# Kernel tuning notes

Hardware: AMD Instinct MI355X
Metric: run time of the kernel (lower is better)

## Reference

```python
import jax, jax.numpy as jnp
import numpy as np

N_HEADS = 16
HEAD_DIM = 64
ROPE_BASE = 10000.0


def _apply_rope(x, offset):
    # x: (B, T, H, hd); rotates consecutive pairs (x[2i], x[2i+1]) as complex numbers,
    # matching torch.view_as_complex on reshape(..., -1, 2).
    B, T, H, hd = x.shape
    inv_freq = 1.0 / (ROPE_BASE ** (jnp.arange(0, hd, 2, dtype=jnp.float32) / hd))  # (hd/2,)
    t = jnp.arange(T, dtype=jnp.float32) + offset
    ang = t[:, None] * inv_freq[None, :]                      # (T, hd/2)
    cos = jnp.cos(ang)[None, :, None, :]                      # (1, T, 1, hd/2)
    sin = jnp.sin(ang)[None, :, None, :]
    x1 = x[..., 0::2]
    x2 = x[..., 1::2]
    out = jnp.stack([x1 * cos - x2 * sin, x1 * sin + x2 * cos], axis=-1)
    return out.reshape(B, T, H, hd).astype(x.dtype)


def setup_inputs() -> dict:
    key = jax.random.key(0)
    ks = jax.random.split(key, 5)
    D = N_HEADS * HEAD_DIM  # 1024
    s = 1.0 / np.sqrt(D)
    x = jax.random.normal(ks[0], (2, 2048, D), jnp.float32)
    Wqkv = jax.random.normal(ks[1], (D, 3 * D), jnp.float32) * s
    bqkv = jax.random.normal(ks[2], (3 * D,), jnp.float32) * 0.01
    Wout = jax.random.normal(ks[3], (D, D), jnp.float32) * s
    bout = jax.random.normal(ks[4], (D,), jnp.float32) * 0.01
    return {"x": x, "Wqkv": Wqkv, "bqkv": bqkv, "Wout": Wout, "bout": bout, "offset": 0}


def reference(x, Wqkv, bqkv, Wout, bout, offset):
    B, T, D = x.shape
    qkv = (x @ Wqkv + bqkv).reshape(B, T, 3, N_HEADS, HEAD_DIM)
    q, k, v = qkv[:, :, 0], qkv[:, :, 1], qkv[:, :, 2]       # (B, T, H, hd)
    q = _apply_rope(q, offset)
    k = _apply_rope(k, offset)
    # kv_cache is None and T == window_size, so no crop occurs.
    new_cache = jnp.stack([k, v], axis=1)                     # (B, 2, T, H, hd)
    scale = 1.0 / np.sqrt(HEAD_DIM)
    scores = jnp.einsum("bqhd,bkhd->bhqk", q, k) * scale      # (B, H, T, T)
    mask = jnp.tril(jnp.ones((T, T), dtype=bool))
    scores = jnp.where(mask[None, None], scores, jnp.finfo(scores.dtype).min)
    attn = jax.nn.softmax(scores, axis=-1)
    ctx = jnp.einsum("bhqk,bkhd->bqhd", attn, v).reshape(B, T, D)
    out = ctx @ Wout + bout
    return (out, new_cache)
```

## Files before the change

### kernel.cpp

```cpp
#include <hip/hip_runtime.h>
#include <stdint.h>
#include <math.h>


typedef __bf16 bf16_t;
typedef bf16_t bf16x8 __attribute__((ext_vector_type(8)));
typedef float f32x4 __attribute__((ext_vector_type(4)));
typedef unsigned short ushort8_t __attribute__((ext_vector_type(8)));

__device__ __forceinline__ unsigned short f2bf(float f) {
    union { float f; unsigned int i; } v; v.f = f;
    unsigned int r = v.i + 0x7fffu + ((v.i >> 16) & 1u);
    return (unsigned short)(r >> 16);
}
__device__ __forceinline__ bf16x8 ld8(const unsigned short* p) {
    return *(const bf16x8*)p;
}
__device__ __forceinline__ void gload_lds16(const unsigned short* g, unsigned short* l) {
    __builtin_amdgcn_global_load_lds(
        (__attribute__((address_space(1))) void*)(g),
        (__attribute__((address_space(3))) void*)(l),
        16, 0, 0);
}
#define WAITN(n) asm volatile("s_waitcnt vmcnt(" #n ")" ::: "memory")

__global__ void k_cvt(const float* __restrict__ in, unsigned short* __restrict__ out) {
    const int i = (blockIdx.x * 256 + threadIdx.x) * 8;
    float4 a = *(const float4*)&in[i];
    float4 b = *(const float4*)&in[i + 4];
    ushort8_t v;
    v[0] = f2bf(a.x); v[1] = f2bf(a.y); v[2] = f2bf(a.z); v[3] = f2bf(a.w);
    v[4] = f2bf(b.x); v[5] = f2bf(b.y); v[6] = f2bf(b.z); v[7] = f2bf(b.w);
    *(ushort8_t*)&out[i] = v;
}

__global__ void k_ropetab(float* __restrict__ tab, const int* __restrict__ offp) {
    int idx = blockIdx.x * blockDim.x + threadIdx.x;
    int t = idx >> 5, i = idx & 31;
    float off = (float)(*offp);
    float inv = powf(10000.0f, -(float)(2 * i) / 64.0f);
    float ang = ((float)t + off) * inv;
    float s, c;
    sincosf(ang, &s, &c);
    tab[idx * 2]     = c;
    tab[idx * 2 + 1] = s;
}

__global__ void k_transposeF2B(const float* __restrict__ in,
                               unsigned short* __restrict__ out, int R, int C) {
    __shared__ __align__(16) float tile[64 * 68];
    const int bz = blockIdx.z;
    const size_t base = (size_t)bz * R * C;
    const int tR = blockIdx.y * 64, tC = blockIdx.x * 64;
    const int tid = threadIdx.x;
#pragma unroll
    for (int it = 0; it < 4; ++it) {
        int flat = (it * 256 + tid) * 4;
        int r = flat >> 6, c = flat & 63;
        *(float4*)&tile[r * 68 + c] =
            *(const float4*)&in[base + (size_t)(tR + r) * C + tC + c];
    }
    __syncthreads();
#pragma unroll
    for (int it = 0; it < 2; ++it) {
        int flat = (it * 256 + tid) * 8;
        int rr = flat >> 6, cc = flat & 63;
        ushort8_t v;
#pragma unroll
        for (int j = 0; j < 8; ++j) v[j] = f2bf(tile[(cc + j) * 68 + rr]);
        *(ushort8_t*)&out[base + (size_t)(tC + rr) * R + tR + cc] = v;
    }
}

__global__ void k_transpose64(const unsigned short* __restrict__ in,
                              unsigned short* __restrict__ out, int R, int C) {
    __shared__ __align__(16) unsigned short tile[64 * 72];
    const int bz = blockIdx.z;
    const size_t base = (size_t)bz * R * C;
    const int tR = blockIdx.y * 64, tC = blockIdx.x * 64;
    const int tid = threadIdx.x;
#pragma unroll
    for (int it = 0; it < 2; ++it) {
        int flat = (it * 256 + tid) * 8;
        int r = flat >> 6, c = flat & 63;
        *(ushort8_t*)&tile[r * 72 + c] =
            *(const ushort8_t*)&in[base + (size_t)(tR + r) * C + tC + c];
    }
    __syncthreads();
#pragma unroll
    for (int it = 0; it < 2; ++it) {
        int flat = (it * 256 + tid) * 8;
        int rr = flat >> 6, cc = flat & 63;
        ushort8_t v;
#pragma unroll
        for (int j = 0; j < 8; ++j) v[j] = tile[(cc + j) * 72 + rr];
        *(ushort8_t*)&out[base + (size_t)(tC + rr) * R + tR + cc] = v;
    }
}

template <int EPI>
__global__ __launch_bounds__(512, 2) void k_gemm(
    const unsigned short* __restrict__ A,
    const unsigned short* __restrict__ Bt,
    const float* __restrict__ bias,
    const float* __restrict__ tab,
    unsigned short* __restrict__ oq,
    unsigned short* __restrict__ ok,
    unsigned short* __restrict__ ov,
    float* __restrict__ cache,
    float* __restrict__ outp)
{
    constexpr int K = 1024;
    __shared__ __align__(16) unsigned short lds[65536];
    unsigned short* lA = lds;
    unsigned short* lB = lds + 32768;

    const int tid  = threadIdx.x;
    const int lane = tid & 63, w = tid >> 6;
    const int wr = w >> 2, wc = w & 3;
    const int lrow = lane & 15, quad = lane >> 4;

    const int gx  = gridDim.x;
    const int nwg = gx * gridDim.y;
    const int bid = blockIdx.y * gx + blockIdx.x;
    const int sw  = (bid & 7) * (nwg >> 3) + (bid >> 3);
    const int blockM = (sw / gx) * 256;
    const int blockN = (sw % gx) * 256;

    const int q8    = (lane & 7) ^ (lane >> 3);
    const int srow0 = ((w * 16 + (lane >> 3)) << 1) + ((q8 >> 2) & 1);
    const int scol  = (q8 & 3) * 8;
    const unsigned short* srcA = A  + (size_t)(blockM + srow0) * K + scol;
    const unsigned short* srcB = Bt + (size_t)(blockN + srow0) * K + scol;
    unsigned short* dA = lA + w * 1024;
    unsigned short* dB = lB + w * 1024;

    const int rp   = lrow >> 1;
    const int swzu = ((((lane & 1) << 6) | (quad << 4)) ^ (rp << 4)) >> 1;

    f32x4 acc[8][4];
#pragma unroll
    for (int m = 0; m < 8; ++m)
#pragma unroll
        for (int n = 0; n < 4; ++n) acc[m][n] = (f32x4){0.f, 0.f, 0.f, 0.f};

#define STAGE_A(T, KH) do { \
        const unsigned short* s_ = srcA + (T) * 64 + (KH) * 32; \
        unsigned short* d_ = dA + (((2*(T)+(KH)) & 3) << 13); \
        gload_lds16(s_, d_); \
        gload_lds16(s_ + 16 * K, d_ + 512); } while (0)
#define STAGE_B(T, KH) do { \
        const unsigned short* s_ = srcB + (T) * 64 + (KH) * 32; \
        unsigned short* d_ = dB + (((2*(T)+(KH)) & 3) << 13); \
        gload_lds16(s_, d_); \
        gload_lds16(s_ + 16 * K, d_ + 512); } while (0)
#define RD_A(slot) do { \
        _Pragma("unroll") \
        for (int m = 0; m < 8; ++m) \
            aA[m] = ld8(&lA[((slot) << 13) + (wr * 64 + m * 8 + rp) * 64 + swzu]); } while (0)
#define RD_B(slot, nh) do { \
        _Pragma("unroll") \
        for (int nl = 0; nl < 2; ++nl) \
            bB[nl] = ld8(&lB[((slot) << 13) + (wc * 32 + (nh) * 16 + nl * 8 + rp) * 64 + swzu]); } while (0)
#define MFMA16(nh) do { \
        __builtin_amdgcn_s_barrier(); \
        asm volatile("s_waitcnt lgkmcnt(0)" ::: "memory"); \
        __builtin_amdgcn_sched_barrier(0); \
        __builtin_amdgcn_s_setprio(1); \
        _Pragma("unroll") \
        for (int m = 0; m < 8; ++m) { \
            acc[m][(nh)*2+0] = __builtin_amdgcn_mfma_f32_16x16x32_bf16(aA[m], bB[0], acc[m][(nh)*2+0], 0, 0, 0); \
            acc[m][(nh)*2+1] = __builtin_amdgcn_mfma_f32_16x16x32_bf16(aA[m], bB[1], acc[m][(nh)*2+1], 0, 0, 0); } \
        __builtin_amdgcn_s_setprio(0); \
        __builtin_amdgcn_s_barrier(); } while (0)

    STAGE_A(0, 0); STAGE_B(0, 0);
    STAGE_A(0, 1); STAGE_B(0, 1);
    STAGE_A(1, 0); STAGE_B(1, 0);
    STAGE_A(1, 1);
    WAITN(8);
    __builtin_amdgcn_s_barrier();

    bf16x8 aA[8], bB[2];
    for (int i = 0; i < 7; ++i) {
        const int E = 2 * i, O = 2 * i + 1;
        WAITN(6); RD_A(0); RD_B(0, 0); STAGE_B(O, 1);     MFMA16(0);
        RD_B(0, 1);                    STAGE_A(E + 2, 0); MFMA16(1);
        RD_A(1); RD_B(1, 0);           STAGE_B(E + 2, 0); MFMA16(0);
        RD_B(1, 1);                    STAGE_A(E + 2, 1); MFMA16(1);
        WAITN(6); RD_A(2); RD_B(2, 0); STAGE_B(E + 2, 1); MFMA16(0);
        RD_B(2, 1);                    STAGE_A(O + 2, 0); MFMA16(1);
        RD_A(3); RD_B(3, 0);           STAGE_B(O + 2, 0); MFMA16(0);
        RD_B(3, 1);                    STAGE_A(O + 2, 1); MFMA16(1);
    }
    WAITN(6); RD_A(0); RD_B(0, 0); STAGE_B(15, 1); MFMA16(0);
    RD_B(0, 1);                                    MFMA16(1);
    RD_A(1); RD_B(1, 0);                           MFMA16(0);
    RD_B(1, 1);                                    MFMA16(1);
    WAITN(0); RD_A(2); RD_B(2, 0);                 MFMA16(0);
    RD_B(2, 1);                                    MFMA16(1);
    RD_A(3); RD_B(3, 0);                           MFMA16(0);
    RD_B(3, 1);                                    MFMA16(1);
#undef STAGE_A
#undef STAGE_B
#undef RD_A
#undef RD_B
#undef MFMA16

#pragma unroll
    for (int m = 0; m < 8; ++m) {
        const int rbase = blockM + wr * 128 + m * 16 + quad * 4;
#pragma unroll
        for (int n = 0; n < 4; ++n) {
            const int gcol = blockN + wc * 64 + n * 16 + lrow;
            const float bv = bias[gcol];
#pragma unroll
            for (int r = 0; r < 4; ++r) {
                const int row = rbase + r;
                float val = acc[m][n][r] + bv;
                if (EPI == 0) {
                    outp[(size_t)row * 1024 + gcol] = val;
                } else {
                    const int s = gcol >> 10;
                    const int cn = gcol & 1023;
                    const int h = cn >> 6, d = cn & 63;
                    const int b = row >> 11, t = row & 2047;
                    if (s < 2) {
                        const int ii = d >> 1;
                        const float cz = tab[t * 64 + 2 * ii];
                        const float sz = tab[t * 64 + 2 * ii + 1];
                        const float pv = __shfl_xor(val, 1);
                        val = (d & 1) ? (pv * sz + val * cz) : (val * cz - pv * sz);
                    }
                    const unsigned short r16 = f2bf(val);
                    const size_t bhtd = (((size_t)(b * 16 + h)) * 2048 + t) * 64 + d;
                    if (s == 0) {
                        oq[bhtd] = r16;
                    } else if (s == 1) {
                        ok[bhtd] = r16;
                        cache[(((size_t)(b * 2 + 0)) * 2048 + t) * 1024 + h * 64 + d] = val;
                    } else {
                        ov[bhtd] = r16;
                        cache[(((size_t)(b * 2 + 1)) * 2048 + t) * 1024 + h * 64 + d] = val;
                    }
                }
            }
        }
    }
}

__global__ __launch_bounds__(256) void k_gemm0(
    const unsigned short* __restrict__ A,
    const unsigned short* __restrict__ Bt,
    const float* __restrict__ bias,
    float* __restrict__ outp)
{
    constexpr int K = 1024;
    __shared__ __align__(16) unsigned short lA[2][64 * 32];
    __shared__ __align__(16) unsigned short lB[2][64 * 32];
    const int tid = threadIdx.x;
    const int wave = tid >> 6, lane = tid & 63;
    const int lrow = lane & 15, quad = lane >> 4;
    const int waveM = wave >> 1, waveN = wave & 1;
    const int blockM = blockIdx.y * 64, blockN = blockIdx.x * 64;

    f32x4 acc[2][2];
#pragma unroll
    for (int i = 0; i < 2; ++i)
#pragma unroll
        for (int j = 0; j < 2; ++j) acc[i][j] = (f32x4){0.f, 0.f, 0.f, 0.f};

    const int srow = tid >> 2;
    const int scol = (tid & 3) * 8;
    auto stage = [&](int k0, int bsel) {
        gload_lds16(&A[(size_t)(blockM + srow) * K + k0 + scol], &lA[bsel][tid * 8]);
        gload_lds16(&Bt[(size_t)(blockN + srow) * K + k0 + scol], &lB[bsel][tid * 8]);
    };

    stage(0, 0);
    int buf = 0;
    for (int k0 = 0; k0 < K; k0 += 32) {
        __syncthreads();
        if (k0 + 32 < K) stage(k0 + 32, buf ^ 1);
        bf16x8 af[2], bfr[2];
#pragma unroll
        for (int mt = 0; mt < 2; ++mt)
            af[mt] = ld8(&lA[buf][(waveM * 32 + mt * 16 + lrow) * 32 + quad * 8]);
#pragma unroll
        for (int nt = 0; nt < 2; ++nt)
            bfr[nt] = ld8(&lB[buf][(waveN * 32 + nt * 16 + lrow) * 32 + quad * 8]);
#pragma unroll
        for (int mt = 0; mt < 2; ++mt)
#pragma unroll
            for (int nt = 0; nt < 2; ++nt)
                acc[mt][nt] = __builtin_amdgcn_mfma_f32_16x16x32_bf16(
                    af[mt], bfr[nt], acc[mt][nt], 0, 0, 0);
        buf ^= 1;
    }

#pragma unroll
    for (int mt = 0; mt < 2; ++mt) {
        const int rbase = blockM + waveM * 32 + mt * 16 + quad * 4;
#pragma unroll
        for (int nt = 0; nt < 2; ++nt) {
            const int gcol = blockN + waveN * 32 + nt * 16 + lrow;
            const float bv = bias[gcol];
#pragma unroll
            for (int r = 0; r < 4; ++r)
                outp[(size_t)(rbase + r) * 1024 + gcol] = acc[mt][nt][r] + bv;
        }
    }
}

__global__ __launch_bounds__(512, 2) void k_attn(
    const unsigned short* __restrict__ qh,
    const unsigned short* __restrict__ kh,
    const unsigned short* __restrict__ vt,
    unsigned short* __restrict__ ctx)
{
    __shared__ __align__(16) unsigned short lK[4][64 * 64];
    __shared__ __align__(16) unsigned short lV[4][64 * 64];
    __shared__ __align__(16) unsigned short lP[8][32 * 68];
    const int tid = threadIdx.x;
    const int wave = tid >> 6, lane = tid & 63;
    const int lrow = lane & 15, quad = lane >> 4;
    const int sub = lane >> 3, g8 = lane & 7;
    const int grp = g8 ^ (sub & 7);
    const int pj = blockIdx.x;
    const int h = blockIdx.y, b = blockIdx.z;
    const unsigned short* Q  = qh + (size_t)(b * 16 + h) * 2048 * 64;
    const unsigned short* Kp = kh + (size_t)(b * 16 + h) * 2048 * 64;
    const unsigned short* Vt = vt + (size_t)(b * 16 + h) * 64 * 2048;

    const int grpq = wave >> 2;
    const int wv   = wave & 3;
    const int qb   = grpq ? pj : (15 - pj);
    const int qw   = qb * 128 + wv * 32;
    const int nT   = 2 * (16 - pj);

    bf16x8 bOnes;
#pragma unroll
    for (int j = 0; j < 8; ++j) bOnes[j] = (bf16_t)1.0f;

    bf16x8 aQ[2][2];
#pragma unroll
    for (int mf = 0; mf < 2; ++mf)
#pragma unroll
        for (int ks = 0; ks < 2; ++ks) {
            bf16x8 t = ld8(&Q[(size_t)(qw + mf * 16 + lrow) * 64 + ks * 32 + quad * 8]);
#pragma unroll
            for (int j = 0; j < 8; ++j) t[j] = (bf16_t)((float)t[j] * 0.125f);
            aQ[mf][ks] = t;
        }

    f32x4 o[2][4];
#pragma unroll
    for (int mf = 0; mf < 2; ++mf)
#pragma unroll
        for (int i = 0; i < 4; ++i) o[mf][i] = (f32x4){0.f, 0.f, 0.f, 0.f};
    f32x4 lacc[2];
    lacc[0] = (f32x4){0.f, 0.f, 0.f, 0.f};
    lacc[1] = (f32x4){0.f, 0.f, 0.f, 0.f};

#define STAGE_T(t) do { \
        const int c_ = wave, s_ = (t) & 3; \
        gload_lds16(&Kp[(size_t)((t) * 64 + c_ * 8 + sub) * 64 + grp * 8], &lK[s_][c_ * 512]); \
        gload_lds16(&Vt[(size_t)(c_ * 8 + sub) * 2048 + (t) * 64 + grp * 8], &lV[s_][c_ * 512]); } while (0)

    STAGE_T(0);
    STAGE_T(1);

    for (int it = 0; it < nT; ++it) {
        if (it + 2 < nT) {
            STAGE_T(it + 2);
            WAITN(4);
        } else if (it + 1 < nT) {
            WAITN(2);
        } else {
            WAITN(0);
        }
        __builtin_amdgcn_s_barrier();
        __builtin_amdgcn_sched_barrier(0);
        const int kt0 = it * 64;
        if (kt0 < qw + 32) {
            const unsigned short* lKb = lK[it & 3];
            const unsigned short* lVb = lV[it & 3];
            f32x4 s[2][4];
#pragma unroll
            for (int mf = 0; mf < 2; ++mf)
#pragma unroll
                for (int i = 0; i < 4; ++i) s[mf][i] = (f32x4){0.f, 0.f, 0.f, 0.f};
            __builtin_amdgcn_s_setprio(1);
#pragma unroll
            for (int nt = 0; nt < 4; ++nt) {
                const int row = nt * 16 + lrow;
#pragma unroll
                for (int ks = 0; ks < 2; ++ks) {
                    bf16x8 bK = ld8(&lKb[row * 64 + (((ks * 4 + quad) ^ (row & 7)) * 8)]);
#pragma unroll
                    for (int mf = 0; mf < 2; ++mf)
                        s[mf][nt] = __builtin_amdgcn_mfma_f32_16x16x32_bf16(
                            aQ[mf][ks], bK, s[mf][nt], 0, 0, 0);
                }
            }
            __builtin_amdgcn_s_setprio(0);
            if (kt0 + 63 > qw) {
#pragma unroll
                for (int mf = 0; mf < 2; ++mf)
#pragma unroll
                    for (int nt = 0; nt < 4; ++nt) {
                        const int colg = kt0 + nt * 16 + lrow;
#pragma unroll
                        for (int r = 0; r < 4; ++r) {
                            const int rowg = qw + mf * 16 + quad * 4 + r;
                            const float pv = (colg <= rowg) ? __expf(s[mf][nt][r]) : 0.f;
                            lP[wave][(mf * 16 + quad * 4 + r) * 68 + nt * 16 + lrow] = f2bf(pv);
                        }
                    }
            } else {
#pragma unroll
                for (int mf = 0; mf < 2; ++mf)
#pragma unroll
                    for (int nt = 0; nt < 4; ++nt)
#pragma unroll
                        for (int r = 0; r < 4; ++r)
                            lP[wave][(mf * 16 + quad * 4 + r) * 68 + nt * 16 + lrow] =
                                f2bf(__expf(s[mf][nt][r]));
            }
            bf16x8 aP[2][2];
#pragma unroll
            for (int mf = 0; mf < 2; ++mf)
#pragma unroll
                for (int ks = 0; ks < 2; ++ks)
                    aP[mf][ks] = ld8(&lP[wave][(mf * 16 + lrow) * 68 + ks * 32 + quad * 8]);
            __builtin_amdgcn_s_setprio(1);
#pragma unroll
            for (int mf = 0; mf < 2; ++mf)
#pragma unroll
                for (int ks = 0; ks < 2; ++ks)
                    lacc[mf] = __builtin_amdgcn_mfma_f32_16x16x32_bf16(
                        aP[mf][ks], bOnes, lacc[mf], 0, 0, 0);
#pragma unroll
            for (int dt = 0; dt < 4; ++dt) {
                const int row = dt * 16 + lrow;
#pragma unroll
                for (int ks = 0; ks < 2; ++ks) {
                    bf16x8 bV = ld8(&lVb[row * 64 + (((ks * 4 + quad) ^ (row & 7)) * 8)]);
#pragma unroll
                    for (int mf = 0; mf < 2; ++mf)
                        o[mf][dt] = __builtin_amdgcn_mfma_f32_16x16x32_bf16(
                            aP[mf][ks], bV, o[mf][dt], 0, 0, 0);
                }
            }
            __builtin_amdgcn_s_setprio(0);
        }
    }
#undef STAGE_T

    float inv[2][4];
#pragma unroll
    for (int mf = 0; mf < 2; ++mf)
#pragma unroll
        for (int r = 0; r < 4; ++r) inv[mf][r] = 1.0f / lacc[mf][r];
#pragma unroll
    for (int mf = 0; mf < 2; ++mf)
#pragma unroll
        for (int dt = 0; dt < 4; ++dt) {
            const int col = h * 64 + dt * 16 + lrow;
#pragma unroll
            for (int r = 0; r < 4; ++r) {
                const int trow = qw + mf * 16 + quad * 4 + r;
                ctx[((size_t)(b * 2048 + trow)) * 1024 + col] = f2bf(o[mf][dt][r] * inv[mf][r]);
            }
        }
}

extern "C" void kernel_launch(void* const* d_in, const int* in_sizes, int n_in,
                              void* d_out, int out_size, void* d_ws, size_t ws_size,
                              hipStream_t stream) {
    (void)in_sizes; (void)n_in; (void)out_size; (void)ws_size;
    const float* x    = (const float*)d_in[0];
    const float* wqkv = (const float*)d_in[1];
    const float* bqkv = (const float*)d_in[2];
    const float* wout = (const float*)d_in[3];
    const float* bout = (const float*)d_in[4];
    const int*   offp = (const int*)d_in[5];

    float* out   = (float*)d_out;
    float* cache = out + (size_t)2 * 2048 * 1024;

    char* w = (char*)d_ws;
    float* tab            = (float*)w;          w += (size_t)2048 * 64 * sizeof(float);
    unsigned short* xb    = (unsigned short*)w; w += (size_t)4194304 * 2;
    unsigned short* wqkvT = (unsigned short*)w; w += (size_t)3072 * 1024 * 2;
    unsigned short* woutT = (unsigned short*)w; w += (size_t)1024 * 1024 * 2;
    unsigned short* qh    = (unsigned short*)w; w += (size_t)4194304 * 2;
    unsigned short* kh    = (unsigned short*)w; w += (size_t)4194304 * 2;
    unsigned short* vh    = (unsigned short*)w; w += (size_t)4194304 * 2;
    unsigned short* vt    = (unsigned short*)w; w += (size_t)4194304 * 2;
    unsigned short* ctx   = (unsigned short*)w; w += (size_t)4194304 * 2;

    k_ropetab<<<dim3(256), dim3(256), 0, stream>>>(tab, offp);
    k_cvt<<<dim3(2048), dim3(256), 0, stream>>>(x, xb);
    k_transposeF2B<<<dim3(48, 16, 1), dim3(256), 0, stream>>>(wqkv, wqkvT, 1024, 3072);
    k_transposeF2B<<<dim3(16, 16, 1), dim3(256), 0, stream>>>(wout, woutT, 1024, 1024);
    k_gemm<1><<<dim3(12, 16), dim3(512), 0, stream>>>(xb, wqkvT, bqkv, tab, qh, kh, vh, cache, nullptr);
    k_transpose64<<<dim3(1, 32, 32), dim3(256), 0, stream>>>(vh, vt, 2048, 64);
    k_attn<<<dim3(8, 16, 2), dim3(512), 0, stream>>>(qh, kh, vt, ctx);
    k_gemm0<<<dim3(16, 64), dim3(256), 0, stream>>>(ctx, woutT, bout, out);
}
```

Baseline: 243.1 us.

## Halve barriers in GEMM main loop and drop MFMA priority boosts

Restructures the LDS pipeline synchronization in the QKV/out GEMM kernel. Previously each MFMA block was bracketed by two s_barriers; now there is one barrier per step, placed before the LDS reads, with the waitcnt moved to the end of each half-iteration. The s_setprio raise around the MFMA block is removed. This is meant to cut barrier stalls, but it relies on a single barrier still protecting LDS slot reuse against the async global-to-LDS writes, which raises a race risk.

```diff
diff --git a/kernel.cpp b/kernel.cpp
--- a/kernel.cpp
+++ b/kernel.cpp
@@ -162,49 +162,49 @@
         _Pragma("unroll") \
         for (int nl = 0; nl < 2; ++nl) \
             bB[nl] = ld8(&lB[((slot) << 13) + (wc * 32 + (nh) * 16 + nl * 8 + rp) * 64 + swzu]); } while (0)
+#define BAR __builtin_amdgcn_s_barrier()
+#define LGKSB do { \
+        asm volatile("s_waitcnt lgkmcnt(0)" ::: "memory"); \
+        __builtin_amdgcn_sched_barrier(0); } while (0)
 #define MFMA16(nh) do { \
-        __builtin_amdgcn_s_barrier(); \
-        asm volatile("s_waitcnt lgkmcnt(0)" ::: "memory"); \
-        __builtin_amdgcn_sched_barrier(0); \
-        __builtin_amdgcn_s_setprio(1); \
         _Pragma("unroll") \
         for (int m = 0; m < 8; ++m) { \
             acc[m][(nh)*2+0] = __builtin_amdgcn_mfma_f32_16x16x32_bf16(aA[m], bB[0], acc[m][(nh)*2+0], 0, 0, 0); \
             acc[m][(nh)*2+1] = __builtin_amdgcn_mfma_f32_16x16x32_bf16(aA[m], bB[1], acc[m][(nh)*2+1], 0, 0, 0); } \
-        __builtin_amdgcn_s_setprio(0); \
-        __builtin_amdgcn_s_barrier(); } while (0)
+        } while (0)
 
     STAGE_A(0, 0); STAGE_B(0, 0);
     STAGE_A(0, 1); STAGE_B(0, 1);
     STAGE_A(1, 0); STAGE_B(1, 0);
     STAGE_A(1, 1);
-    WAITN(8);
-    __builtin_amdgcn_s_barrier();
+    WAITN(6);
 
     bf16x8 aA[8], bB[2];
     for (int i = 0; i < 7; ++i) {
         const int E = 2 * i, O = 2 * i + 1;
-        WAITN(6); RD_A(0); RD_B(0, 0); STAGE_B(O, 1);     MFMA16(0);
-        RD_B(0, 1);                    STAGE_A(E + 2, 0); MFMA16(1);
-        RD_A(1); RD_B(1, 0);           STAGE_B(E + 2, 0); MFMA16(0);
-        RD_B(1, 1);                    STAGE_A(E + 2, 1); MFMA16(1);
-        WAITN(6); RD_A(2); RD_B(2, 0); STAGE_B(E + 2, 1); MFMA16(0);
-        RD_B(2, 1);                    STAGE_A(O + 2, 0); MFMA16(1);
-        RD_A(3); RD_B(3, 0);           STAGE_B(O + 2, 0); MFMA16(0);
-        RD_B(3, 1);                    STAGE_A(O + 2, 1); MFMA16(1);
-    }
-    WAITN(6); RD_A(0); RD_B(0, 0); STAGE_B(15, 1); MFMA16(0);
-    RD_B(0, 1);                                    MFMA16(1);
-    RD_A(1); RD_B(1, 0);                           MFMA16(0);
-    RD_B(1, 1);                                    MFMA16(1);
-    WAITN(0); RD_A(2); RD_B(2, 0);                 MFMA16(0);
-    RD_B(2, 1);                                    MFMA16(1);
-    RD_A(3); RD_B(3, 0);                           MFMA16(0);
-    RD_B(3, 1);                                    MFMA16(1);
+        BAR; RD_A(0); RD_B(0, 0); STAGE_B(O, 1);     LGKSB; MFMA16(0);
+        BAR; RD_B(0, 1);          STAGE_A(E + 2, 0); LGKSB; MFMA16(1);
+        BAR; RD_A(1); RD_B(1, 0); STAGE_B(E + 2, 0); LGKSB; MFMA16(0);
+        BAR; RD_B(1, 1);          STAGE_A(E + 2, 1); LGKSB; MFMA16(1); WAITN(6);
+        BAR; RD_A(2); RD_B(2, 0); STAGE_B(E + 2, 1); LGKSB; MFMA16(0);
+        BAR; RD_B(2, 1);          STAGE_A(O + 2, 0); LGKSB; MFMA16(1);
+        BAR; RD_A(3); RD_B(3, 0); STAGE_B(O + 2, 0); LGKSB; MFMA16(0);
+        BAR; RD_B(3, 1);          STAGE_A(O + 2, 1); LGKSB; MFMA16(1); WAITN(6);
+    }
+    BAR; RD_A(0); RD_B(0, 0); STAGE_B(15, 1); LGKSB; MFMA16(0);
+    BAR; RD_B(0, 1);                          LGKSB; MFMA16(1);
+    BAR; RD_A(1); RD_B(1, 0);                 LGKSB; MFMA16(0);
+    BAR; RD_B(1, 1);                          LGKSB; MFMA16(1); WAITN(0);
+    BAR; RD_A(2); RD_B(2, 0);                 LGKSB; MFMA16(0);
+    BAR; RD_B(2, 1);                          LGKSB; MFMA16(1);
+    BAR; RD_A(3); RD_B(3, 0);                 LGKSB; MFMA16(0);
+    BAR; RD_B(3, 1);                          LGKSB; MFMA16(1);
 #undef STAGE_A
 #undef STAGE_B
 #undef RD_A
 #undef RD_B
+#undef BAR
+#undef LGKSB
 #undef MFMA16
 
 #pragma unroll
```

New measurement: 243.8 us. About the same (+0.3%).
